# Performance work log

Hardware: AMD Instinct MI355X
Metric: run time of the kernel (lower is better)

The kernel has to match this reference:

```python
import jax, jax.numpy as jnp
import numpy as np

B, S, H = 2, 2048, 1024
NH, NKV, HD = 16, 4, 64

def setup_inputs() -> dict:
    key = jax.random.key(0)
    k1, k2, k3, k4, k5 = jax.random.split(key, 5)
    return {
        "hidden_states": jax.random.normal(k1, (B, S, H), dtype=jnp.float32),
        "attention_mask": jnp.ones((B, S), dtype=jnp.int32),
        "wq": jax.random.normal(k2, (H, NH * HD), dtype=jnp.float32) * 0.02,
        "wk": jax.random.normal(k3, (H, NKV * HD), dtype=jnp.float32) * 0.02,
        "wv": jax.random.normal(k4, (H, NKV * HD), dtype=jnp.float32) * 0.02,
        "wo": jax.random.normal(k5, (NH * HD, 1), dtype=jnp.float32) * 0.02,
    }

def reference(hidden_states, attention_mask, wq, wk, wv, wo):
    bsz, seq_len, _ = hidden_states.shape
    n_rep = NH // NKV
    # projections -> (b, h, s, d)
    q = (hidden_states @ wq).reshape(bsz, seq_len, NH, HD).transpose(0, 2, 1, 3)
    k = (hidden_states @ wk).reshape(bsz, seq_len, NKV, HD).transpose(0, 2, 1, 3)
    v = (hidden_states @ wv).reshape(bsz, seq_len, NKV, HD).transpose(0, 2, 1, 3)
    # repeat_kv == repeat_interleave along head axis
    k = jnp.repeat(k, n_rep, axis=1)
    v = jnp.repeat(v, n_rep, axis=1)
    scores = jnp.einsum('bhqd,bhkd->bhqk', q, k) / np.sqrt(HD).astype(np.float32)
    mask = attention_mask[:, None, None, :]  # (b,1,1,k)
    scores = jnp.where(mask == 0, jnp.float32(-jnp.inf), scores)
    attn = jax.nn.softmax(scores, axis=-1)
    out = jnp.einsum('bhqk,bhkd->bqhd', attn, v).reshape(bsz, seq_len, NH * HD)
    return out @ wo  # (b, s, 1)
```

## Files before the change

kernel.cpp:

```cpp
#include <hip/hip_runtime.h>
#include <stdint.h>


typedef __bf16 bf16x8 __attribute__((ext_vector_type(8)));
typedef float f32x4 __attribute__((ext_vector_type(4)));

__device__ inline unsigned short f2bf(float f) {
    unsigned int u = __builtin_bit_cast(unsigned int, f);
    u += 0x7fff + ((u >> 16) & 1);
    return (unsigned short)(u >> 16);
}
__device__ inline bf16x8 ldfrag(const unsigned short* p) {
    uint4 v = *(const uint4*)p;
    return __builtin_bit_cast(bf16x8, v);
}
__device__ inline void gl2lds16(const unsigned short* g, unsigned short* l) {
    __builtin_amdgcn_global_load_lds(
        (const __attribute__((address_space(1))) void*)g,
        (__attribute__((address_space(3))) void*)l, 16, 0, 0);
}

#define SCALE_Q 0.18033688011112042f

__global__ __launch_bounds__(256) void prep_kernel(
    const float* __restrict__ hs, const float* __restrict__ wq,
    const float* __restrict__ wk, const float* __restrict__ wv,
    const float* __restrict__ wo,
    unsigned short* __restrict__ hs_bf, unsigned short* __restrict__ wT)
{
    int bid = blockIdx.x, tid = threadIdx.x;
    if (bid < 4096) {
        int u = bid * 256 + tid;
        float4 v = ((const float4*)hs)[u];
        ushort4 o;
        o.x = f2bf(v.x); o.y = f2bf(v.y); o.z = f2bf(v.z); o.w = f2bf(v.w);
        ((ushort4*)hs_bf)[u] = o;
    } else if (bid < 4416) {
        __shared__ float tile[64 * 65];
        int t = bid - 4096;
        int ntile = t / 16, ctile = t % 16;
        int nb = ntile * 64, cb = ctile * 64;
        int tx = tid & 63, ty = tid >> 6;
        for (int i = 0; i < 16; i++) {
            int cl = i * 4 + ty;
            int n = nb + tx;
            float v = (n < 1024) ? wq[(cb + cl) * 1024 + n] * SCALE_Q
                                 : wk[(cb + cl) * 256 + (n - 1024)];
            tile[cl * 65 + tx] = v;
        }
        __syncthreads();
        for (int i = 0; i < 16; i++) {
            int nl = i * 4 + ty;
            wT[(nb + nl) * 1024 + cb + tx] = f2bf(tile[tx * 65 + nl]);
        }
    } else {
        int u = (bid - 4416) * 256 + tid;
        int n2 = u >> 10, c = u & 1023;
        if (n2 < 16) {
            int h = n2, kv = h >> 2;
            const float* wvr = wv + c * 256 + kv * 64;
            const float* wor = wo + h * 64;
            float s = 0.f;
            #pragma unroll 8
            for (int d = 0; d < 64; d++) s += wvr[d] * wor[d];
            wT[(1280 + n2) * 1024 + c] = f2bf(s);
        } else {
            wT[(1280 + n2) * 1024 + c] = 0;
        }
    }
}

__global__ __launch_bounds__(256) void gemm_kernel(
    const unsigned short* __restrict__ hs_bf, const unsigned short* __restrict__ wT,
    unsigned short* __restrict__ Qp, unsigned short* __restrict__ Kp,
    float* __restrict__ vproj)
{
    __shared__ __align__(16) unsigned short Al[128 * 32];
    __shared__ __align__(16) unsigned short Bl[128 * 32];
    int nt = blockIdx.x, rt = blockIdx.y;
    int tid = threadIdx.x;
    int lane = tid & 63, w = tid >> 6;
    int l15 = lane & 15, quad = lane >> 4;
    int wm = (w >> 1) * 64, wn = (w & 1) * 64;

    f32x4 acc[4][4];
    const f32x4 zero = {0.f, 0.f, 0.f, 0.f};
    for (int i = 0; i < 4; i++) for (int j = 0; j < 4; j++) acc[i][j] = zero;

    int arow = nt * 128, rrow = rt * 128;
    int srow = w * 32 + (lane >> 2);
    int scol = (lane & 3) * 8;
    const unsigned short* ga = wT    + (size_t)(arow + srow) * 1024 + scol;
    const unsigned short* gb = hs_bf + (size_t)(rrow + srow) * 1024 + scol;
    unsigned short* la = Al + (w * 32) * 32;
    unsigned short* lb = Bl + (w * 32) * 32;

    for (int kk = 0; kk < 32; kk++) {
        gl2lds16(ga,             la);
        gl2lds16(ga + 16 * 1024, la + 16 * 32);
        gl2lds16(gb,             lb);
        gl2lds16(gb + 16 * 1024, lb + 16 * 32);
        ga += 32; gb += 32;
        __syncthreads();
        bf16x8 af[4], bfr[4];
        for (int i = 0; i < 4; i++) {
            af[i]  = ldfrag(Al + (wm + i * 16 + l15) * 32 + quad * 8);
            bfr[i] = ldfrag(Bl + (wn + i * 16 + l15) * 32 + quad * 8);
        }
        for (int i = 0; i < 4; i++)
            for (int j = 0; j < 4; j++)
                acc[i][j] = __builtin_amdgcn_mfma_f32_16x16x32_bf16(af[i], bfr[j], acc[i][j], 0, 0, 0);
        __syncthreads();
    }

    for (int i = 0; i < 4; i++) {
        for (int j = 0; j < 4; j++) {
            int nw = nt * 128 + wm + i * 16 + quad * 4;
            int r  = rt * 128 + wn + j * 16 + l15;
            if (nt < 8) {
                ushort4 o;
                o.x = f2bf(acc[i][j][0]); o.y = f2bf(acc[i][j][1]);
                o.z = f2bf(acc[i][j][2]); o.w = f2bf(acc[i][j][3]);
                *(ushort4*)(Qp + (size_t)r * 1024 + nw) = o;
            } else if (nt < 10) {
                ushort4 o;
                o.x = f2bf(acc[i][j][0]); o.y = f2bf(acc[i][j][1]);
                o.z = f2bf(acc[i][j][2]); o.w = f2bf(acc[i][j][3]);
                *(ushort4*)(Kp + (size_t)r * 256 + (nw - 1024)) = o;
            } else {
                for (int rg = 0; rg < 4; rg++) {
                    int h = nw + rg - 1280;
                    if (h < 16)
                        vproj[((size_t)(r >> 11) * 16 + h) * 2048 + (r & 2047)] = acc[i][j][rg];
                }
            }
        }
    }
}

__global__ __launch_bounds__(256) void attn_kernel(
    const unsigned short* __restrict__ Qp, const unsigned short* __restrict__ Kp,
    const float* __restrict__ vproj, const int* __restrict__ mask,
    float2* __restrict__ part)
{
    __shared__ __align__(16) unsigned short Kl[256 * 80];
    __shared__ __align__(16) float vpml[4 * 256];
    __shared__ __align__(16) float biasl[256];
    int qt = blockIdx.x;
    int b = blockIdx.y >> 2, kv = blockIdx.y & 3;
    int ks = blockIdx.z;
    int tid = threadIdx.x, lane = tid & 63, w = tid >> 6;
    int l15 = lane & 15, quad = lane >> 4;
    int h = kv * 4 + w;
    int k0 = ks * 256;
    int qrow0 = qt * 64;

    bf16x8 qf[4][2];
    for (int qs = 0; qs < 4; qs++) {
        const unsigned short* qp =
            Qp + (size_t)(b * 2048 + qrow0 + qs * 16 + l15) * 1024 + h * 64 + quad * 8;
        qf[qs][0] = ldfrag(qp);
        qf[qs][1] = ldfrag(qp + 32);
    }

    for (int it = 0; it < 8; it++) {
        int u = it * 256 + tid;
        int row = u >> 3, ch = u & 7;
        *(uint4*)(Kl + row * 80 + ch * 8) =
            *(const uint4*)(Kp + (size_t)(b * 2048 + k0 + row) * 256 + kv * 64 + ch * 8);
    }
    {
        int h2 = tid >> 6, kk = (tid & 63) * 4;
        *(float4*)(vpml + h2 * 256 + kk) =
            *(const float4*)(vproj + ((size_t)b * 16 + kv * 4 + h2) * 2048 + k0 + kk);
    }
    if (tid < 64) {
        int4 mm = *(const int4*)(mask + b * 2048 + k0 + tid * 4);
        float4 bb;
        bb.x = mm.x ? 0.f : -30000.f;
        bb.y = mm.y ? 0.f : -30000.f;
        bb.z = mm.z ? 0.f : -30000.f;
        bb.w = mm.w ? 0.f : -30000.f;
        *(float4*)(biasl + tid * 4) = bb;
    }
    __syncthreads();

    float num[4] = {0.f, 0.f, 0.f, 0.f}, den[4] = {0.f, 0.f, 0.f, 0.f};
    for (int t8 = 0; t8 < 16; t8++) {
        const unsigned short* kb = Kl + (t8 * 16 + l15) * 80 + quad * 8;
        bf16x8 a0 = ldfrag(kb);
        bf16x8 a1 = ldfrag(kb + 32);
        f32x4 vpm4 = *(const f32x4*)(vpml + w * 256 + t8 * 16 + quad * 4);
        f32x4 c4   = *(const f32x4*)(biasl + t8 * 16 + quad * 4);
        for (int qs = 0; qs < 4; qs++) {
            f32x4 d = __builtin_amdgcn_mfma_f32_16x16x32_bf16(a0, qf[qs][0], c4, 0, 0, 0);
            d = __builtin_amdgcn_mfma_f32_16x16x32_bf16(a1, qf[qs][1], d, 0, 0, 0);
            for (int r = 0; r < 4; r++) {
                float e = __builtin_amdgcn_exp2f(d[r]);
                num[qs] += e * vpm4[r];
                den[qs] += e;
            }
        }
    }
    for (int qs = 0; qs < 4; qs++) {
        float n = num[qs], dd = den[qs];
        n += __shfl_xor(n, 16);  n += __shfl_xor(n, 32);
        dd += __shfl_xor(dd, 16); dd += __shfl_xor(dd, 32);
        if (quad == 0) {
            int q = qrow0 + qs * 16 + l15;
            part[((size_t)(b * 2048 + q) * 16 + h) * 8 + ks] = make_float2(n, dd);
        }
    }
}

__global__ __launch_bounds__(256) void combine_kernel(
    const float2* __restrict__ part, float* __restrict__ out)
{
    int wid = (blockIdx.x * 256 + threadIdx.x) >> 6;
    int lane = threadIdx.x & 63;
    const float2* base = part + (size_t)wid * 128;
    float2 p0 = base[lane];
    float2 p1 = base[64 + lane];
    for (int m = 1; m <= 4; m <<= 1) {
        p0.x += __shfl_xor(p0.x, m); p0.y += __shfl_xor(p0.y, m);
        p1.x += __shfl_xor(p1.x, m); p1.y += __shfl_xor(p1.y, m);
    }
    float v = p0.x / p0.y + p1.x / p1.y;
    for (int m = 8; m <= 32; m <<= 1) v += __shfl_xor(v, m);
    if (lane == 0) out[wid] = v;
}

extern "C" void kernel_launch(void* const* d_in, const int* in_sizes, int n_in,
                              void* d_out, int out_size, void* d_ws, size_t ws_size,
                              hipStream_t stream)
{
    const float* hs  = (const float*)d_in[0];
    const int* mask  = (const int*)d_in[1];
    const float* wq  = (const float*)d_in[2];
    const float* wk  = (const float*)d_in[3];
    const float* wv  = (const float*)d_in[4];
    const float* wo  = (const float*)d_in[5];

    char* ws = (char*)d_ws;
    unsigned short* hs_bf = (unsigned short*)ws;
    unsigned short* wT    = (unsigned short*)(ws + 8388608);
    unsigned short* Qp    = (unsigned short*)(ws + 11272192);
    unsigned short* Kp    = (unsigned short*)(ws + 19660800);
    float* vproj          = (float*)(ws + 21757952);
    float2* part          = (float2*)(ws + 22020096);

    prep_kernel<<<4928, 256, 0, stream>>>(hs, wq, wk, wv, wo, hs_bf, wT);
    gemm_kernel<<<dim3(11, 32), 256, 0, stream>>>(hs_bf, wT, Qp, Kp, vproj);
    attn_kernel<<<dim3(32, 8, 8), 256, 0, stream>>>(Qp, Kp, vproj, mask, part);
    combine_kernel<<<1024, 256, 0, stream>>>(part, (float*)d_out);
}
```

Measured before the change: 147.1 us.

## Fuse combine into attention via full-key loop and atomics; double-buffer GEMM LDS

The attention kernel now processes all 2048 keys per block, looping over eight K tiles of 256 instead of splitting keys across grid z. It reduces the per-head ratios in shared memory and atomically adds them into the output, which is zeroed by extra blocks in the prep kernel, so the separate combine kernel and the partials buffer are gone. Query tiles shrink to 32 rows to keep enough blocks. Separately, the GEMM double-buffers its LDS tiles so the next global-to-LDS load is issued before computing on the current one. The trade-offs are fewer blocks (512 vs 2048) with serialized K loads, and non-deterministic float atomic ordering.

```diff
diff --git a/kernel.cpp b/kernel.cpp
--- a/kernel.cpp
+++ b/kernel.cpp
@@ -26,7 +26,8 @@
     const float* __restrict__ hs, const float* __restrict__ wq,
     const float* __restrict__ wk, const float* __restrict__ wv,
     const float* __restrict__ wo,
-    unsigned short* __restrict__ hs_bf, unsigned short* __restrict__ wT)
+    unsigned short* __restrict__ hs_bf, unsigned short* __restrict__ wT,
+    float* __restrict__ out)
 {
     int bid = blockIdx.x, tid = threadIdx.x;
     if (bid < 4096) {
@@ -53,7 +54,7 @@
             int nl = i * 4 + ty;
             wT[(nb + nl) * 1024 + cb + tx] = f2bf(tile[tx * 65 + nl]);
         }
-    } else {
+    } else if (bid < 4928) {
         int u = (bid - 4416) * 256 + tid;
         int n2 = u >> 10, c = u & 1023;
         if (n2 < 16) {
@@ -67,6 +68,10 @@
         } else {
             wT[(1280 + n2) * 1024 + c] = 0;
         }
+    } else {
+        int u = (bid - 4928) * 256 + tid;
+        float4 z = {0.f, 0.f, 0.f, 0.f};
+        ((float4*)out)[u] = z;
     }
 }
 
@@ -75,8 +80,8 @@
     unsigned short* __restrict__ Qp, unsigned short* __restrict__ Kp,
     float* __restrict__ vproj)
 {
-    __shared__ __align__(16) unsigned short Al[128 * 32];
-    __shared__ __align__(16) unsigned short Bl[128 * 32];
+    __shared__ __align__(16) unsigned short Al[2][128 * 32];
+    __shared__ __align__(16) unsigned short Bl[2][128 * 32];
     int nt = blockIdx.x, rt = blockIdx.y;
     int tid = threadIdx.x;
     int lane = tid & 63, w = tid >> 6;
@@ -92,20 +97,28 @@
     int scol = (lane & 3) * 8;
     const unsigned short* ga = wT    + (size_t)(arow + srow) * 1024 + scol;
     const unsigned short* gb = hs_bf + (size_t)(rrow + srow) * 1024 + scol;
-    unsigned short* la = Al + (w * 32) * 32;
-    unsigned short* lb = Bl + (w * 32) * 32;
+    int lofs = (w * 32) * 32;
+
+    gl2lds16(ga,             Al[0] + lofs);
+    gl2lds16(ga + 16 * 1024, Al[0] + lofs + 16 * 32);
+    gl2lds16(gb,             Bl[0] + lofs);
+    gl2lds16(gb + 16 * 1024, Bl[0] + lofs + 16 * 32);
+    ga += 32; gb += 32;
+    __syncthreads();
 
     for (int kk = 0; kk < 32; kk++) {
-        gl2lds16(ga,             la);
-        gl2lds16(ga + 16 * 1024, la + 16 * 32);
-        gl2lds16(gb,             lb);
-        gl2lds16(gb + 16 * 1024, lb + 16 * 32);
-        ga += 32; gb += 32;
-        __syncthreads();
+        int cur = kk & 1, nxt = cur ^ 1;
+        if (kk < 31) {
+            gl2lds16(ga,             Al[nxt] + lofs);
+            gl2lds16(ga + 16 * 1024, Al[nxt] + lofs + 16 * 32);
+            gl2lds16(gb,             Bl[nxt] + lofs);
+            gl2lds16(gb + 16 * 1024, Bl[nxt] + lofs + 16 * 32);
+            ga += 32; gb += 32;
+        }
         bf16x8 af[4], bfr[4];
         for (int i = 0; i < 4; i++) {
-            af[i]  = ldfrag(Al + (wm + i * 16 + l15) * 32 + quad * 8);
-            bfr[i] = ldfrag(Bl + (wn + i * 16 + l15) * 32 + quad * 8);
+            af[i]  = ldfrag(Al[cur] + (wm + i * 16 + l15) * 32 + quad * 8);
+            bfr[i] = ldfrag(Bl[cur] + (wn + i * 16 + l15) * 32 + quad * 8);
         }
         for (int i = 0; i < 4; i++)
             for (int j = 0; j < 4; j++)
@@ -141,22 +154,20 @@
 __global__ __launch_bounds__(256) void attn_kernel(
     const unsigned short* __restrict__ Qp, const unsigned short* __restrict__ Kp,
     const float* __restrict__ vproj, const int* __restrict__ mask,
-    float2* __restrict__ part)
+    float* __restrict__ out)
 {
     __shared__ __align__(16) unsigned short Kl[256 * 80];
-    __shared__ __align__(16) float vpml[4 * 256];
-    __shared__ __align__(16) float biasl[256];
+    __shared__ __align__(16) float vpml[4 * 2048];
+    __shared__ __align__(16) float biasl[2048];
     int qt = blockIdx.x;
     int b = blockIdx.y >> 2, kv = blockIdx.y & 3;
-    int ks = blockIdx.z;
     int tid = threadIdx.x, lane = tid & 63, w = tid >> 6;
     int l15 = lane & 15, quad = lane >> 4;
     int h = kv * 4 + w;
-    int k0 = ks * 256;
-    int qrow0 = qt * 64;
-
-    bf16x8 qf[4][2];
-    for (int qs = 0; qs < 4; qs++) {
+    int qrow0 = qt * 32;
+
+    bf16x8 qf[2][2];
+    for (int qs = 0; qs < 2; qs++) {
         const unsigned short* qp =
             Qp + (size_t)(b * 2048 + qrow0 + qs * 16 + l15) * 1024 + h * 64 + quad * 8;
         qf[qs][0] = ldfrag(qp);
@@ -165,69 +176,63 @@
 
     for (int it = 0; it < 8; it++) {
         int u = it * 256 + tid;
-        int row = u >> 3, ch = u & 7;
-        *(uint4*)(Kl + row * 80 + ch * 8) =
-            *(const uint4*)(Kp + (size_t)(b * 2048 + k0 + row) * 256 + kv * 64 + ch * 8);
-    }
-    {
-        int h2 = tid >> 6, kk = (tid & 63) * 4;
-        *(float4*)(vpml + h2 * 256 + kk) =
-            *(const float4*)(vproj + ((size_t)b * 16 + kv * 4 + h2) * 2048 + k0 + kk);
-    }
-    if (tid < 64) {
-        int4 mm = *(const int4*)(mask + b * 2048 + k0 + tid * 4);
+        int h2 = u >> 9, kk = (u & 511) * 4;
+        *(float4*)(vpml + h2 * 2048 + kk) =
+            *(const float4*)(vproj + ((size_t)b * 16 + kv * 4 + h2) * 2048 + kk);
+    }
+    for (int it = 0; it < 2; it++) {
+        int idx = (it * 256 + tid) * 4;
+        int4 mm = *(const int4*)(mask + b * 2048 + idx);
         float4 bb;
         bb.x = mm.x ? 0.f : -30000.f;
         bb.y = mm.y ? 0.f : -30000.f;
         bb.z = mm.z ? 0.f : -30000.f;
         bb.w = mm.w ? 0.f : -30000.f;
-        *(float4*)(biasl + tid * 4) = bb;
-    }
+        *(float4*)(biasl + idx) = bb;
+    }
+
+    float num[2] = {0.f, 0.f}, den[2] = {0.f, 0.f};
+    for (int ks = 0; ks < 8; ks++) {
+        __syncthreads();
+        for (int it = 0; it < 8; it++) {
+            int u = it * 256 + tid;
+            int row = u >> 3, ch = u & 7;
+            *(uint4*)(Kl + row * 80 + ch * 8) =
+                *(const uint4*)(Kp + (size_t)(b * 2048 + ks * 256 + row) * 256 + kv * 64 + ch * 8);
+        }
+        __syncthreads();
+
+        for (int t8 = 0; t8 < 16; t8++) {
+            const unsigned short* kb = Kl + (t8 * 16 + l15) * 80 + quad * 8;
+            bf16x8 a0 = ldfrag(kb);
+            bf16x8 a1 = ldfrag(kb + 32);
+            f32x4 vpm4 = *(const f32x4*)(vpml + w * 2048 + ks * 256 + t8 * 16 + quad * 4);
+            f32x4 c4   = *(const f32x4*)(biasl + ks * 256 + t8 * 16 + quad * 4);
+            for (int qs = 0; qs < 2; qs++) {
+                f32x4 d = __builtin_amdgcn_mfma_f32_16x16x32_bf16(a0, qf[qs][0], c4, 0, 0, 0);
+                d = __builtin_amdgcn_mfma_f32_16x16x32_bf16(a1, qf[qs][1], d, 0, 0, 0);
+                for (int r = 0; r < 4; r++) {
+                    float e = __builtin_amdgcn_exp2f(d[r]);
+                    num[qs] += e * vpm4[r];
+                    den[qs] += e;
+                }
+            }
+        }
+    }
+
     __syncthreads();
-
-    float num[4] = {0.f, 0.f, 0.f, 0.f}, den[4] = {0.f, 0.f, 0.f, 0.f};
-    for (int t8 = 0; t8 < 16; t8++) {
-        const unsigned short* kb = Kl + (t8 * 16 + l15) * 80 + quad * 8;
-        bf16x8 a0 = ldfrag(kb);
-        bf16x8 a1 = ldfrag(kb + 32);
-        f32x4 vpm4 = *(const f32x4*)(vpml + w * 256 + t8 * 16 + quad * 4);
-        f32x4 c4   = *(const f32x4*)(biasl + t8 * 16 + quad * 4);
-        for (int qs = 0; qs < 4; qs++) {
-            f32x4 d = __builtin_amdgcn_mfma_f32_16x16x32_bf16(a0, qf[qs][0], c4, 0, 0, 0);
-            d = __builtin_amdgcn_mfma_f32_16x16x32_bf16(a1, qf[qs][1], d, 0, 0, 0);
-            for (int r = 0; r < 4; r++) {
-                float e = __builtin_amdgcn_exp2f(d[r]);
-                num[qs] += e * vpm4[r];
-                den[qs] += e;
-            }
-        }
-    }
-    for (int qs = 0; qs < 4; qs++) {
+    float* vsum = (float*)Kl;
+    for (int qs = 0; qs < 2; qs++) {
         float n = num[qs], dd = den[qs];
         n += __shfl_xor(n, 16);  n += __shfl_xor(n, 32);
         dd += __shfl_xor(dd, 16); dd += __shfl_xor(dd, 32);
-        if (quad == 0) {
-            int q = qrow0 + qs * 16 + l15;
-            part[((size_t)(b * 2048 + q) * 16 + h) * 8 + ks] = make_float2(n, dd);
-        }
-    }
-}
-
-__global__ __launch_bounds__(256) void combine_kernel(
-    const float2* __restrict__ part, float* __restrict__ out)
-{
-    int wid = (blockIdx.x * 256 + threadIdx.x) >> 6;
-    int lane = threadIdx.x & 63;
-    const float2* base = part + (size_t)wid * 128;
-    float2 p0 = base[lane];
-    float2 p1 = base[64 + lane];
-    for (int m = 1; m <= 4; m <<= 1) {
-        p0.x += __shfl_xor(p0.x, m); p0.y += __shfl_xor(p0.y, m);
-        p1.x += __shfl_xor(p1.x, m); p1.y += __shfl_xor(p1.y, m);
-    }
-    float v = p0.x / p0.y + p1.x / p1.y;
-    for (int m = 8; m <= 32; m <<= 1) v += __shfl_xor(v, m);
-    if (lane == 0) out[wid] = v;
+        if (quad == 0) vsum[w * 32 + qs * 16 + l15] = n / dd;
+    }
+    __syncthreads();
+    if (tid < 32) {
+        float v = vsum[tid] + vsum[32 + tid] + vsum[64 + tid] + vsum[96 + tid];
+        atomicAdd(out + b * 2048 + qrow0 + tid, v);
+    }
 }
 
 extern "C" void kernel_launch(void* const* d_in, const int* in_sizes, int n_in,
@@ -247,10 +252,8 @@
     unsigned short* Qp    = (unsigned short*)(ws + 11272192);
     unsigned short* Kp    = (unsigned short*)(ws + 19660800);
     float* vproj          = (float*)(ws + 21757952);
-    float2* part          = (float2*)(ws + 22020096);
-
-    prep_kernel<<<4928, 256, 0, stream>>>(hs, wq, wk, wv, wo, hs_bf, wT);
+
+    prep_kernel<<<4932, 256, 0, stream>>>(hs, wq, wk, wv, wo, hs_bf, wT, (float*)d_out);
     gemm_kernel<<<dim3(11, 32), 256, 0, stream>>>(hs_bf, wT, Qp, Kp, vproj);
-    attn_kernel<<<dim3(32, 8, 8), 256, 0, stream>>>(Qp, Kp, vproj, mask, part);
-    combine_kernel<<<1024, 256, 0, stream>>>(part, (float*)d_out);
-}
+    attn_kernel<<<dim3(64, 8), 256, 0, stream>>>(Qp, Kp, vproj, mask, (float*)d_out);
+}
```

Result: slower. 157.5 us (+7.1%).
